# Kernel optimization log

Measured on AMD Instinct MI355X. Metric: run time of the kernel, lower is better.

The kernel has to match this reference:

```python
import jax, jax.numpy as jnp
import numpy as np

B, S, D = 4, 2048, 1024
NH, NKV = 16, 4
HD = D // NH  # 64


def _rope(x, freqs):
    # x: [B, H, S, HD], freqs: [B, S, HD//2]
    cos = jnp.concatenate([jnp.cos(freqs), jnp.cos(freqs)], axis=-1)[:, None]  # [B,1,S,HD]
    sin = jnp.concatenate([jnp.sin(freqs), jnp.sin(freqs)], axis=-1)[:, None]
    x1, x2 = x[..., : HD // 2], x[..., HD // 2:]
    rot = jnp.concatenate([-x2, x1], axis=-1)
    return x * cos + rot * sin


def setup_inputs() -> dict:
    key = jax.random.key(0)
    ks = jax.random.split(key, 9)
    return {
        "hidden_states": jax.random.normal(ks[0], (B, S, D), jnp.float32),
        "rotary_pos_emb": jax.random.normal(ks[1], (B, S, HD // 2), jnp.float32),
        "Wq": jax.random.normal(ks[2], (D, NH * HD), jnp.float32) * 0.02,
        "bq": jax.random.normal(ks[3], (NH * HD,), jnp.float32) * 0.02,
        "Wk": jax.random.normal(ks[4], (D, NKV * HD), jnp.float32) * 0.02,
        "bk": jax.random.normal(ks[5], (NKV * HD,), jnp.float32) * 0.02,
        "Wv": jax.random.normal(ks[6], (D, NKV * HD), jnp.float32) * 0.02,
        "bv": jax.random.normal(ks[7], (NKV * HD,), jnp.float32) * 0.02,
        "Wo": jax.random.normal(ks[8], (NH * HD, D), jnp.float32) * 0.02,
    }


def reference(hidden_states, rotary_pos_emb, Wq, bq, Wk, bk, Wv, bv, Wo):
    b, s, _ = hidden_states.shape
    # projections -> [B, H, S, HD]
    q = (hidden_states @ Wq + bq).reshape(b, s, NH, HD).transpose(0, 2, 1, 3)
    k = (hidden_states @ Wk + bk).reshape(b, s, NKV, HD).transpose(0, 2, 1, 3)
    v = (hidden_states @ Wv + bv).reshape(b, s, NKV, HD).transpose(0, 2, 1, 3)
    q = _rope(q, rotary_pos_emb)
    k = _rope(k, rotary_pos_emb)
    groups = NH // NKV
    k = jnp.repeat(k, groups, axis=1)  # [B, NH, S, HD]
    v = jnp.repeat(v, groups, axis=1)
    scaling = HD ** -0.5
    scores = jnp.einsum("bhqd,bhkd->bhqk", q, k) * scaling
    probs = jax.nn.softmax(scores.astype(jnp.float32), axis=-1).astype(q.dtype)
    out = jnp.einsum("bhqk,bhkd->bhqd", probs, v)
    out = out.transpose(0, 2, 1, 3).reshape(b, s, NH * HD)
    return out @ Wo
```

## Files before the change

kernel.cpp:

```cpp
#include <hip/hip_runtime.h>
#include <hip/hip_bf16.h>

#define BB 4
#define SS 2048
#define DD 1024
#define NH 16
#define NKV 4
#define HD 64
#define MROWS (BB*SS)
#define NQKV (NH*HD + 2*NKV*HD)
#define KOFF (NH*HD)

typedef short v8s __attribute__((ext_vector_type(8)));
typedef short v4s __attribute__((ext_vector_type(4)));
typedef float v4f __attribute__((ext_vector_type(4)));
typedef unsigned short u16;
typedef unsigned int u32;

__device__ __forceinline__ float bf2f(u16 u){
  union { float f; u32 i; } x; x.i = ((u32)u) << 16; return x.f;
}
__device__ __forceinline__ u16 f2bf(float f){
  union { __hip_bfloat16 h; u16 u; } x; x.h = __float2bfloat16(f); return x.u;
}
__device__ __forceinline__ u32 cvtpk(float lo, float hi){
  u32 r;
  asm("v_cvt_pk_bf16_f32 %0, %1, %2" : "=v"(r) : "v"(lo), "v"(hi));
  return r;
}
__device__ __forceinline__ float fmax3(float a, float b, float c){
  return fmaxf(fmaxf(a, b), c);
}
__device__ __forceinline__ void gl_lds16(const u16* g, u16* l){
  __builtin_amdgcn_global_load_lds(
      (const __attribute__((address_space(1))) u32*)g,
      (__attribute__((address_space(3))) u32*)l, 16, 0, 0);
}


__global__ void cast_x(const float* __restrict__ in, u16* __restrict__ out, int n4){
  int i = blockIdx.x*256 + threadIdx.x;
  if (i >= n4) return;
  float4 v = reinterpret_cast<const float4*>(in)[i];
  ushort4 o;
  o.x = f2bf(v.x); o.y = f2bf(v.y); o.z = f2bf(v.z); o.w = f2bf(v.w);
  reinterpret_cast<ushort4*>(out)[i] = o;
}

__global__ void build_bqkv(const float* __restrict__ Wq, const float* __restrict__ Wk,
                           const float* __restrict__ Wv, const float* __restrict__ bq,
                           const float* __restrict__ bk, const float* __restrict__ bv,
                           u16* __restrict__ Bt, float* __restrict__ bias){
  __shared__ float T[32][33];
  const int kt = blockIdx.x*32, nt = blockIdx.y*32;
  const int tx = threadIdx.x, ty = threadIdx.y;
  const int n = nt + tx;
  const float* src; int ld, nb;
  if (nt < 1024)      { src = Wq; ld = 1024; nb = n; }
  else if (nt < 1280) { src = Wk; ld = 256;  nb = n - 1024; }
  else                { src = Wv; ld = 256;  nb = n - 1280; }
  #pragma unroll
  for (int i=0;i<4;i++)
    T[ty + 8*i][tx] = src[(long)(kt + ty + 8*i)*ld + nb];
  __syncthreads();
  #pragma unroll
  for (int i=0;i<4;i++)
    Bt[(long)(nt + ty + 8*i)*1024 + kt + tx] = f2bf(T[tx][ty + 8*i]);
  if (blockIdx.x == 0 && ty == 0)
    bias[n] = (n < 1024) ? bq[n] : (n < 1280 ? bk[n-1024] : bv[n-1280]);
}

__global__ void build_wo(const float* __restrict__ Wo, u16* __restrict__ Bt){
  __shared__ float T[32][33];
  const int kt = blockIdx.x*32, nt = blockIdx.y*32;
  const int tx = threadIdx.x, ty = threadIdx.y;
  #pragma unroll
  for (int i=0;i<4;i++)
    T[ty + 8*i][tx] = Wo[(long)(kt + ty + 8*i)*1024 + nt + tx];
  __syncthreads();
  #pragma unroll
  for (int i=0;i<4;i++)
    Bt[(long)(nt + ty + 8*i)*1024 + kt + tx] = f2bf(T[tx][ty + 8*i]);
}


template<bool BIAS, typename OT>
__global__ __launch_bounds__(256) void gemm_bt(
    const u16* __restrict__ A, const u16* __restrict__ Bt,
    const float* __restrict__ bias, const float* __restrict__ fr,
    OT* __restrict__ C, int K, int ldc)
{
  __shared__ u16 As[128*64];
  __shared__ u16 Bs[128*64];
  const int tid = threadIdx.x;
  const int wid = tid >> 6, lane = tid & 63;
  const int g = lane >> 4, c = lane & 15;
  const long brow = (long)blockIdx.y * 128;
  const long bcol = (long)blockIdx.x * 128;
  const int wr = (wid >> 1) * 64, wc = (wid & 1) * 64;
  const int srow = tid >> 3;
  const int scol = (tid & 7) * 8;
  const u16* ga = &A [(brow + srow)*K + scol];
  const u16* gb = &Bt[(bcol + srow)*K + scol];
  u16* la = &As[(wid*8)*64];
  u16* lb = &Bs[(wid*8)*64];
  v4f acc[4][4] = {};
  for (int kt = 0; kt < K; kt += 64) {
    __syncthreads();
    #pragma unroll
    for (int e = 0; e < 4; ++e) {
      gl_lds16(ga + (long)e*32*K + kt, la + e*32*64);
      gl_lds16(gb + (long)e*32*K + kt, lb + e*32*64);
    }
    __syncthreads();
    #pragma unroll
    for (int ks = 0; ks < 2; ++ks) {
      v8s af[4], bf[4];
      #pragma unroll
      for (int m=0;m<4;m++) af[m] = *reinterpret_cast<const v8s*>(&As[(wr + m*16 + c)*64 + ks*32 + g*8]);
      #pragma unroll
      for (int n=0;n<4;n++) bf[n] = *reinterpret_cast<const v8s*>(&Bs[(wc + n*16 + c)*64 + ks*32 + g*8]);
      __builtin_amdgcn_s_setprio(1);
      #pragma unroll
      for (int m=0;m<4;m++)
        #pragma unroll
        for (int n=0;n<4;n++)
          acc[m][n] = __builtin_amdgcn_mfma_f32_16x16x32_bf16(af[m], bf[n], acc[m][n], 0,0,0);
      __builtin_amdgcn_s_setprio(0);
    }
  }
  const int cb = (int)bcol + wc;
  if (BIAS && cb >= KOFF && cb < KOFF + NKV*HD) {
    #pragma unroll
    for (int m=0;m<4;m++)
      #pragma unroll
      for (int r2=0;r2<4;r2++){
        long row = brow + wr + m*16 + g*4 + r2;
        #pragma unroll
        for (int np=0;np<2;np++){
          int d = np*16 + c;
          int col1 = cb + d, col2 = col1 + 32;
          float v1 = acc[m][np  ][r2] + bias[col1];
          float v2 = acc[m][np+2][r2] + bias[col2];
          float f = fr[row*32 + d];
          float sn, cs; __sincosf(f, &sn, &cs);
          C[row*ldc + col1] = (OT)f2bf(v1*cs - v2*sn);
          C[row*ldc + col2] = (OT)f2bf(v2*cs + v1*sn);
        }
      }
  } else {
    #pragma unroll
    for (int m=0;m<4;m++)
      #pragma unroll
      for (int n=0;n<4;n++) {
        int col = cb + n*16 + c;
        float badd = BIAS ? bias[col] : 0.0f;
        #pragma unroll
        for (int r2=0;r2<4;r2++){
          long row = brow + wr + m*16 + g*4 + r2;
          float v = acc[m][n][r2] + badd;
          if constexpr (sizeof(OT)==2) C[row*ldc + col] = (OT)f2bf(v);
          else                         C[row*ldc + col] = (OT)v;
        }
      }
  }
}


__global__ __launch_bounds__(512) void attn_k(const u16* __restrict__ QKV,
                                              const float* __restrict__ fr,
                                              u16* __restrict__ Out){
  __shared__ u16 Ks[2][64][72];
  __shared__ u16 Vs[2][64][72];
  const int tid = threadIdx.x;
  const int wid = tid >> 6, lane = tid & 63;
  const int g = lane >> 4, c = lane & 15;
  const int qt = blockIdx.x & 7;
  const int bh = blockIdx.x >> 3;
  const int b = bh >> 4, h = bh & 15;
  const int kvh = h >> 2;
  const u16* Qb = QKV + (long)b*SS*NQKV + h*HD;
  const u16* Kb = QKV + (long)b*SS*NQKV + KOFF + kvh*HD;
  const u16* Vb = Kb + NKV*HD;

  const float SCL = 0.125f * 1.44269504088896f;
  v8s qf[2][2];
  #pragma unroll
  for (int qn=0;qn<2;qn++){
    int lrow = qt*256 + wid*32 + qn*16 + c;
    v8s q0 = *reinterpret_cast<const v8s*>(&Qb[(long)lrow*NQKV + g*8]);
    v8s q1 = *reinterpret_cast<const v8s*>(&Qb[(long)lrow*NQKV + 32 + g*8]);
    const float* frp = fr + ((long)b*SS + lrow)*32 + g*8;
    float4 f0 = *reinterpret_cast<const float4*>(frp);
    float4 f1 = *reinterpret_cast<const float4*>(frp + 4);
    float fa[8] = {f0.x,f0.y,f0.z,f0.w,f1.x,f1.y,f1.z,f1.w};
    float r0[8], r1[8];
    #pragma unroll
    for (int j=0;j<8;j++){
      float x1 = bf2f((u16)q0[j]), x2 = bf2f((u16)q1[j]);
      float sn, cs; __sincosf(fa[j], &sn, &cs);
      r0[j] = (x1*cs - x2*sn) * SCL;
      r1[j] = (x2*cs + x1*sn) * SCL;
    }
    union { v8s v; u32 w[4]; } a0, a1;
    #pragma unroll
    for (int wi=0;wi<4;wi++){
      a0.w[wi] = cvtpk(r0[2*wi], r0[2*wi+1]);
      a1.w[wi] = cvtpk(r1[2*wi], r1[2*wi+1]);
    }
    qf[qn][0] = a0.v; qf[qn][1] = a1.v;
  }

  v8s onesf;
  {
    short ov = (c==0) ? (short)0x3F80 : (short)0;
    #pragma unroll
    for (int j=0;j<8;j++) onesf[j] = ov;
  }

  v4f o[2][5] = {};
  float mr[2] = {0.f, 0.f};

  const int krow = tid >> 3;
  const int kcol = (tid & 7) * 8;
  const int key0 = 2*(tid >> 4);
  const int dg4  = (tid & 15) * 4;
  const int slot0 = 32*(key0>>5) + 8*((key0>>2)&3) + 4*((key0>>4)&1) + (key0&3);
  int vofs[4];
  #pragma unroll
  for (int j=0;j<4;j++){
    int d = dg4 + j;
    int idx = (((slot0>>3) ^ (d>>3)) << 3) | (slot0 & 7);
    vofs[j] = d*72 + idx;
  }
  u16* VsF = &Vs[0][0][0];

  const u16* kp  = Kb + (long)krow*NQKV + kcol;
  const u16* vp0 = Vb + (long)key0*NQKV + dg4;
  const u16* vp1 = vp0 + NQKV;

  v8s kreg;
  union { v4s v; u32 w[2]; } vr0, vr1;

  {
    kreg  = *reinterpret_cast<const v8s*>(kp);
    vr0.v = *reinterpret_cast<const v4s*>(vp0);
    vr1.v = *reinterpret_cast<const v4s*>(vp1);
    *reinterpret_cast<v8s*>(&Ks[0][krow][kcol]) = kreg;
    #pragma unroll
    for (int j=0;j<4;j++){
      u32 pkd = __builtin_amdgcn_perm(vr1.w[j>>1], vr0.w[j>>1],
                                      (j&1) ? 0x07060302u : 0x05040100u);
      *reinterpret_cast<u32*>(&VsF[vofs[j]]) = pkd;
    }
  }
  __syncthreads();

  int p = 0;
  for (int t = 0; t < SS/64; ++t){
    if (t+1 < SS/64) {
      long off = (long)(t+1)*64*NQKV;
      kreg  = *reinterpret_cast<const v8s*>(kp  + off);
      vr0.v = *reinterpret_cast<const v4s*>(vp0 + off);
      vr1.v = *reinterpret_cast<const v4s*>(vp1 + off);
    }

    v4f st[4][2];
    #pragma unroll
    for (int qn=0;qn<2;qn++){
      v4f mi = {-mr[qn], -mr[qn], -mr[qn], -mr[qn]};
      #pragma unroll
      for (int km=0;km<4;km++) st[km][qn] = mi;
    }
    #pragma unroll
    for (int ks=0;ks<2;ks++){
      v8s kf[4];
      #pragma unroll
      for (int km=0;km<4;km++)
        kf[km] = *reinterpret_cast<const v8s*>(&Ks[p][km*16 + c][ks*32 + g*8]);
      __builtin_amdgcn_s_setprio(1);
      #pragma unroll
      for (int km=0;km<4;km++)
        #pragma unroll
        for (int qn=0;qn<2;qn++)
          st[km][qn] = __builtin_amdgcn_mfma_f32_16x16x32_bf16(kf[km], qf[qn][ks], st[km][qn], 0,0,0);
      __builtin_amdgcn_s_setprio(0);
    }

    float al[2];
    bool upd[2];
    #pragma unroll
    for (int qn=0;qn<2;qn++){
      float t0 = fmax3(st[0][qn][0], st[0][qn][1], st[0][qn][2]);
      float t1 = fmax3(st[0][qn][3], st[1][qn][0], st[1][qn][1]);
      float t2 = fmax3(st[1][qn][2], st[1][qn][3], st[2][qn][0]);
      float t3 = fmax3(st[2][qn][1], st[2][qn][2], st[2][qn][3]);
      float t4 = fmax3(st[3][qn][0], st[3][qn][1], st[3][qn][2]);
      float mx = fmaxf(fmax3(t0, t1, t2), fmax3(t3, t4, st[3][qn][3]));
      upd[qn] = !__all(mx <= 8.0f);
      al[qn] = 1.0f;
      if (upd[qn]) {
        mx = fmaxf(mx, __shfl_xor(mx, 16));
        mx = fmaxf(mx, __shfl_xor(mx, 32));
        float d = fmaxf(mx, 0.0f);
        al[qn] = __builtin_amdgcn_exp2f(-d);
        mr[qn] += d;
        #pragma unroll
        for (int km=0;km<4;km++)
          #pragma unroll
          for (int r2=0;r2<4;r2++)
            st[km][qn][r2] -= d;
      }
      #pragma unroll
      for (int km=0;km<4;km++)
        #pragma unroll
        for (int r2=0;r2<4;r2++)
          st[km][qn][r2] = __builtin_amdgcn_exp2f(st[km][qn][r2]);
    }

    v8s pa[2][2];
    #pragma unroll
    for (int qm=0;qm<2;qm++)
      #pragma unroll
      for (int ks=0;ks<2;ks++){
        union { v8s v; u32 w[4]; } u;
        u.w[0] = cvtpk(st[2*ks  ][qm][0], st[2*ks  ][qm][1]);
        u.w[1] = cvtpk(st[2*ks  ][qm][2], st[2*ks  ][qm][3]);
        u.w[2] = cvtpk(st[2*ks+1][qm][0], st[2*ks+1][qm][1]);
        u.w[3] = cvtpk(st[2*ks+1][qm][2], st[2*ks+1][qm][3]);
        pa[qm][ks] = u.v;
      }

    if (upd[0] | upd[1]) {
      #pragma unroll
      for (int qm=0;qm<2;qm++)
        #pragma unroll
        for (int r2=0;r2<4;r2++){
          float a = __shfl(al[qm], g*4 + r2);
          #pragma unroll
          for (int dn=0;dn<5;dn++) o[qm][dn][r2] *= a;
        }
    }

    #pragma unroll
    for (int ks=0;ks<2;ks++){
      __builtin_amdgcn_s_setprio(1);
      #pragma unroll
      for (int dn=0;dn<4;dn++){
        int d0 = dn*16 + c;
        v8s vf = *reinterpret_cast<const v8s*>(&Vs[p][d0][(((ks*4+g) ^ (d0>>3)) << 3)]);
        #pragma unroll
        for (int qm=0;qm<2;qm++)
          o[qm][dn] = __builtin_amdgcn_mfma_f32_16x16x32_bf16(pa[qm][ks], vf, o[qm][dn], 0,0,0);
      }
      #pragma unroll
      for (int qm=0;qm<2;qm++)
        o[qm][4] = __builtin_amdgcn_mfma_f32_16x16x32_bf16(pa[qm][ks], onesf, o[qm][4], 0,0,0);
      __builtin_amdgcn_s_setprio(0);
    }

    if (t+1 < SS/64) {
      *reinterpret_cast<v8s*>(&Ks[p^1][krow][kcol]) = kreg;
      const int bofs = (p^1) * (64*72);
      #pragma unroll
      for (int j=0;j<4;j++){
        u32 pkd = __builtin_amdgcn_perm(vr1.w[j>>1], vr0.w[j>>1],
                                        (j&1) ? 0x07060302u : 0x05040100u);
        *reinterpret_cast<u32*>(&VsF[bofs + vofs[j]]) = pkd;
      }
    }
    __syncthreads();
    p ^= 1;
  }

  #pragma unroll
  for (int qm=0;qm<2;qm++)
    #pragma unroll
    for (int r2=0;r2<4;r2++){
      float l = __shfl(o[qm][4][r2], lane & 48);
      float inv = 1.0f / l;
      long row = (long)b*SS + qt*256 + wid*32 + qm*16 + g*4 + r2;
      #pragma unroll
      for (int dn=0;dn<4;dn++)
        Out[row*DD + h*HD + dn*16 + c] = f2bf(o[qm][dn][r2] * inv);
    }
}


extern "C" void kernel_launch(void* const* d_in, const int* in_sizes, int n_in,
                              void* d_out, int out_size, void* d_ws, size_t ws_size,
                              hipStream_t stream)
{
  const float* hs = (const float*)d_in[0];
  const float* fr = (const float*)d_in[1];
  const float* Wq = (const float*)d_in[2];
  const float* bq = (const float*)d_in[3];
  const float* Wk = (const float*)d_in[4];
  const float* bk = (const float*)d_in[5];
  const float* Wv = (const float*)d_in[6];
  const float* bv = (const float*)d_in[7];
  const float* Wo = (const float*)d_in[8];
  float* out = (float*)d_out;
  char* ws = (char*)d_ws;

  u16*   Xb   = (u16*)(ws);
  u16*   Bqkv = (u16*)(ws + 16777216);
  u16*   WoT  = (u16*)(ws + 16777216 + 3145728);
  float* bias = (float*)(ws + 16777216 + 3145728 + 2097152);
  u16*   QKV  = (u16*)(ws + 22028288);
  u16*   AO   = (u16*)(ws + 22028288 + 25165824);

  cast_x    <<<8192, 256, 0, stream>>>(hs, Xb, MROWS*DD/4);
  build_bqkv<<<dim3(32,48), dim3(32,8), 0, stream>>>(Wq, Wk, Wv, bq, bk, bv, Bqkv, bias);
  build_wo  <<<dim3(32,32), dim3(32,8), 0, stream>>>(Wo, WoT);
  gemm_bt<true,  u16>  <<<dim3(NQKV/128, MROWS/128), 256, 0, stream>>>(Xb, Bqkv, bias, fr, QKV, DD, NQKV);
  attn_k    <<<BB*NH*(SS/256), 512, 0, stream>>>(QKV, fr, AO);
  gemm_bt<false, float><<<dim3(DD/128, MROWS/128), 256, 0, stream>>>(AO, WoT, nullptr, nullptr, out, DD, DD);
}
```

Baseline: 181.7 us.

## Precompute rope trig table and apply Q rope and scale in QKV GEMM epilogue

Adds a kernel that precomputes cos/sin pairs for the rotary frequencies into a table stored in the attention-output buffer, which is free until attention runs. The QKV GEMM epilogue now applies RoPE to both Q and K from this table and folds the softmax scale into Q. The attention kernel then loads Q directly without per-element sincos work. This trades one extra small launch and table traffic for removing redundant transcendental work, and Q is now rounded to bf16 after scaling in the GEMM instead of inside attention.

```diff
diff --git a/kernel.cpp b/kernel.cpp
--- a/kernel.cpp
+++ b/kernel.cpp
@@ -45,6 +45,13 @@
   ushort4 o;
   o.x = f2bf(v.x); o.y = f2bf(v.y); o.z = f2bf(v.z); o.w = f2bf(v.w);
   reinterpret_cast<ushort4*>(out)[i] = o;
+}
+
+__global__ void build_trig(const float* __restrict__ fr, float2* __restrict__ trig){
+  int i = blockIdx.x*256 + threadIdx.x;
+  float f = fr[i];
+  float sn, cs; __sincosf(f, &sn, &cs);
+  trig[i] = make_float2(cs, sn);
 }
 
 __global__ void build_bqkv(const float* __restrict__ Wq, const float* __restrict__ Wk,
@@ -87,7 +94,7 @@
 template<bool BIAS, typename OT>
 __global__ __launch_bounds__(256) void gemm_bt(
     const u16* __restrict__ A, const u16* __restrict__ Bt,
-    const float* __restrict__ bias, const float* __restrict__ fr,
+    const float* __restrict__ bias, const float2* __restrict__ trig,
     OT* __restrict__ C, int K, int ldc)
 {
   __shared__ u16 As[128*64];
@@ -130,7 +137,8 @@
     }
   }
   const int cb = (int)bcol + wc;
-  if (BIAS && cb >= KOFF && cb < KOFF + NKV*HD) {
+  if (BIAS && cb < KOFF + NKV*HD) {
+    const float sc = (cb < KOFF) ? 0.125f * 1.44269504088896f : 1.0f;
     #pragma unroll
     for (int m=0;m<4;m++)
       #pragma unroll
@@ -142,10 +150,9 @@
           int col1 = cb + d, col2 = col1 + 32;
           float v1 = acc[m][np  ][r2] + bias[col1];
           float v2 = acc[m][np+2][r2] + bias[col2];
-          float f = fr[row*32 + d];
-          float sn, cs; __sincosf(f, &sn, &cs);
-          C[row*ldc + col1] = (OT)f2bf(v1*cs - v2*sn);
-          C[row*ldc + col2] = (OT)f2bf(v2*cs + v1*sn);
+          float2 t = trig[row*32 + d];
+          C[row*ldc + col1] = (OT)f2bf((v1*t.x - v2*t.y) * sc);
+          C[row*ldc + col2] = (OT)f2bf((v2*t.x + v1*t.y) * sc);
         }
       }
   } else {
@@ -168,7 +175,6 @@
 
 
 __global__ __launch_bounds__(512) void attn_k(const u16* __restrict__ QKV,
-                                              const float* __restrict__ fr,
                                               u16* __restrict__ Out){
   __shared__ u16 Ks[2][64][72];
   __shared__ u16 Vs[2][64][72];
@@ -183,33 +189,13 @@
   const u16* Kb = QKV + (long)b*SS*NQKV + KOFF + kvh*HD;
   const u16* Vb = Kb + NKV*HD;
 
-  const float SCL = 0.125f * 1.44269504088896f;
   v8s qf[2][2];
   #pragma unroll
-  for (int qn=0;qn<2;qn++){
-    int lrow = qt*256 + wid*32 + qn*16 + c;
-    v8s q0 = *reinterpret_cast<const v8s*>(&Qb[(long)lrow*NQKV + g*8]);
-    v8s q1 = *reinterpret_cast<const v8s*>(&Qb[(long)lrow*NQKV + 32 + g*8]);
-    const float* frp = fr + ((long)b*SS + lrow)*32 + g*8;
-    float4 f0 = *reinterpret_cast<const float4*>(frp);
-    float4 f1 = *reinterpret_cast<const float4*>(frp + 4);
-    float fa[8] = {f0.x,f0.y,f0.z,f0.w,f1.x,f1.y,f1.z,f1.w};
-    float r0[8], r1[8];
-    #pragma unroll
-    for (int j=0;j<8;j++){
-      float x1 = bf2f((u16)q0[j]), x2 = bf2f((u16)q1[j]);
-      float sn, cs; __sincosf(fa[j], &sn, &cs);
-      r0[j] = (x1*cs - x2*sn) * SCL;
-      r1[j] = (x2*cs + x1*sn) * SCL;
-    }
-    union { v8s v; u32 w[4]; } a0, a1;
-    #pragma unroll
-    for (int wi=0;wi<4;wi++){
-      a0.w[wi] = cvtpk(r0[2*wi], r0[2*wi+1]);
-      a1.w[wi] = cvtpk(r1[2*wi], r1[2*wi+1]);
-    }
-    qf[qn][0] = a0.v; qf[qn][1] = a1.v;
-  }
+  for (int qn=0;qn<2;qn++)
+    #pragma unroll
+    for (int ks=0;ks<2;ks++)
+      qf[qn][ks] = *reinterpret_cast<const v8s*>(
+        &Qb[(long)(qt*256 + wid*32 + qn*16 + c)*NQKV + ks*32 + g*8]);
 
   v8s onesf;
   {
@@ -409,11 +395,13 @@
   float* bias = (float*)(ws + 16777216 + 3145728 + 2097152);
   u16*   QKV  = (u16*)(ws + 22028288);
   u16*   AO   = (u16*)(ws + 22028288 + 25165824);
+  float2* trig = (float2*)AO;
 
   cast_x    <<<8192, 256, 0, stream>>>(hs, Xb, MROWS*DD/4);
+  build_trig<<<1024, 256, 0, stream>>>(fr, trig);
   build_bqkv<<<dim3(32,48), dim3(32,8), 0, stream>>>(Wq, Wk, Wv, bq, bk, bv, Bqkv, bias);
   build_wo  <<<dim3(32,32), dim3(32,8), 0, stream>>>(Wo, WoT);
-  gemm_bt<true,  u16>  <<<dim3(NQKV/128, MROWS/128), 256, 0, stream>>>(Xb, Bqkv, bias, fr, QKV, DD, NQKV);
-  attn_k    <<<BB*NH*(SS/256), 512, 0, stream>>>(QKV, fr, AO);
+  gemm_bt<true,  u16>  <<<dim3(NQKV/128, MROWS/128), 256, 0, stream>>>(Xb, Bqkv, bias, trig, QKV, DD, NQKV);
+  attn_k    <<<BB*NH*(SS/256), 512, 0, stream>>>(QKV, AO);
   gemm_bt<false, float><<<dim3(DD/128, MROWS/128), 256, 0, stream>>>(AO, WoT, nullptr, nullptr, out, DD, DD);
 }
```

New measurement: 184.8 us. No clear change (+1.7%).
